# Optimization experiments

Measured on AMD Instinct MI355X. Metric: run time of the kernel, lower is better.

Reference implementation:

```python
import math
import jax, jax.numpy as jnp
import numpy as np

B, S, D, H, KV = 2, 2048, 1024, 16, 4
HD = D // H  # 64
ROPE_BASE = 10000.0
RMS_EPS = 1.1920929e-07  # torch.finfo(float32).eps, F.rms_norm default


def setup_inputs() -> dict:
    key = jax.random.key(0)
    ks = jax.random.split(key, 5)
    x = jax.random.normal(ks[0], (B, S, D), jnp.float32)
    Wq = jax.random.normal(ks[1], (D, D), jnp.float32) * 0.02
    Wk = jax.random.normal(ks[2], (KV * HD, D), jnp.float32) * 0.02
    Wv = jax.random.normal(ks[3], (KV * HD, D), jnp.float32) * 0.02
    Wproj = jax.random.normal(ks[4], (D, D), jnp.float32) * 0.02
    q_gain = jnp.ones((H,), jnp.float32)  # qk_gain_init = 1.0
    return {"x": x, "Wq": Wq, "Wk": Wk, "Wv": Wv, "Wproj": Wproj, "q_gain": q_gain}


def _rms_norm(t):
    # F.rms_norm with no weight: t * rsqrt(mean(t^2) + eps)
    return t * jax.lax.rsqrt(jnp.mean(t * t, axis=-1, keepdims=True) + RMS_EPS)


def _rope(t, cos, sin):
    half = t.shape[-1] // 2
    t1, t2 = t[..., :half], t[..., half:]
    return jnp.concatenate([t1 * cos + t2 * sin, t1 * -sin + t2 * cos], axis=-1)


def reference(x, Wq, Wk, Wv, Wproj, q_gain):
    bsz, seqlen, dim = x.shape
    hd = dim // H
    # QKV projections (Linear weight layout [out, in])
    q = (x @ Wq.T).reshape(bsz, seqlen, H, hd).transpose(0, 2, 1, 3)    # [B,H,S,hd]
    k = (x @ Wk.T).reshape(bsz, seqlen, KV, hd).transpose(0, 2, 1, 3)   # [B,KV,S,hd]
    v = (x @ Wv.T).reshape(bsz, seqlen, KV, hd).transpose(0, 2, 1, 3)
    # per-head RMSNorm on q/k (no learned weight)
    q = _rms_norm(q)
    k = _rms_norm(k)
    # RoPE tables
    inv_freq = 1.0 / (ROPE_BASE ** (jnp.arange(0, hd, 2, dtype=jnp.float32) / hd))
    t = jnp.arange(seqlen, dtype=jnp.float32)
    freqs = t[:, None] * inv_freq[None, :]                              # [S, hd/2]
    cos = jnp.cos(freqs)[None, None]                                    # [1,1,S,hd/2]
    sin = jnp.sin(freqs)[None, None]
    q = _rope(q, cos, sin)
    k = _rope(k, cos, sin)
    # learned per-head query gain
    q = q * q_gain[None, :, None, None]
    # GQA: repeat_interleave kv heads to full head count
    rep = H // KV
    k = jnp.repeat(k, rep, axis=1)                                      # [B,H,S,hd]
    v = jnp.repeat(v, rep, axis=1)
    # causal SDPA, scale = 1/sqrt(head_dim)
    scores = jnp.einsum("bhqd,bhkd->bhqk", q, k) * (1.0 / math.sqrt(hd))
    causal = jnp.tril(jnp.ones((seqlen, seqlen), bool))
    scores = jnp.where(causal[None, None], scores, jnp.finfo(scores.dtype).min)
    attn = jax.nn.softmax(scores, axis=-1)
    y = jnp.einsum("bhqk,bhkd->bhqd", attn, v)
    y = y.transpose(0, 2, 1, 3).reshape(bsz, seqlen, dim)
    return y @ Wproj.T
```

## Files before the change

kernel.cpp:

```cpp
#include <hip/hip_runtime.h>

typedef unsigned short u16;
typedef __bf16 bf16_t;
typedef bf16_t bf16x8 __attribute__((ext_vector_type(8)));
typedef float f32x4 __attribute__((ext_vector_type(4)));
typedef u16 u16x8 __attribute__((ext_vector_type(8)));

__device__ __forceinline__ u16 f2bf(float f) {
  unsigned u = __float_as_uint(f);
  u += 0x7fffu + ((u >> 16) & 1u);
  return (u16)(u >> 16);
}

__device__ __forceinline__ unsigned cvtpk(float lo, float hi) {
  unsigned r;
  asm("v_cvt_pk_bf16_f32 %0, %1, %2" : "=v"(r) : "v"(lo), "v"(hi));
  return r;
}

__device__ __forceinline__ f32x4 mfma16(bf16x8 a, bf16x8 b, f32x4 c) {
  return __builtin_amdgcn_mfma_f32_16x16x32_bf16(a, b, c, 0, 0, 0);
}

__device__ __forceinline__ void gl2lds16(const u16* g, u16* l) {
  __builtin_amdgcn_global_load_lds(
      (__attribute__((address_space(1))) void*)(u16*)g,
      (__attribute__((address_space(3))) void*)l, 16, 0, 0);
}

__device__ __forceinline__ void cast8(const float* __restrict__ in,
                                      u16* __restrict__ out, int i) {
  float4 a = *(const float4*)&in[i];
  float4 b = *(const float4*)&in[i + 4];
  uint4 o;
  o.x = cvtpk(a.x, a.y);
  o.y = cvtpk(a.z, a.w);
  o.z = cvtpk(b.x, b.y);
  o.w = cvtpk(b.z, b.w);
  *(uint4*)&out[i] = o;
}

__global__ __launch_bounds__(256) void megacast(
    const float* __restrict__ x, const float* __restrict__ Wq,
    const float* __restrict__ Wk, const float* __restrict__ Wv,
    const float* __restrict__ Wp, u16* __restrict__ xb,
    u16* __restrict__ wallb, u16* __restrict__ wpb,
    float2* __restrict__ tbl) {
  const int blk = blockIdx.x;
  const int tid = threadIdx.x;
  if (blk < 2048) {
    cast8(x, xb, (blk * 256 + tid) * 8);
  } else if (blk < 2560) {
    cast8(Wq, wallb, ((blk - 2048) * 256 + tid) * 8);
  } else if (blk < 2688) {
    cast8(Wk, wallb + 1048576, ((blk - 2560) * 256 + tid) * 8);
  } else if (blk < 2816) {
    cast8(Wv, wallb + 1310720, ((blk - 2688) * 256 + tid) * 8);
  } else if (blk < 3328) {
    cast8(Wp, wpb, ((blk - 2816) * 256 + tid) * 8);
  } else {
    const int idx = (blk - 3328) * 256 + tid;
    const int s = idx >> 5, i = idx & 31;
    float inv = exp2f(-(float)i * (13.287712379549449f / 32.0f));
    float fr = (float)s * inv;
    float sn, cs;
    sincosf(fr, &sn, &cs);
    tbl[idx] = make_float2(cs, sn);
  }
}

template <int BM, int BN, int NTN, bool O16>
__global__ __launch_bounds__(256) void gemm_bt(const u16* __restrict__ A,
                                               const u16* __restrict__ B,
                                               void* __restrict__ Cv,
                                               int M, int N, int K) {
  constexpr int FM = BM / 32;
  constexpr int FN = BN / 32;
  constexpr int NL = (BM + BN) / 32;
  __shared__ __align__(16) u16 As[2][BM][64];
  __shared__ __align__(16) u16 Bs[2][BN][64];
  const int tid = threadIdx.x;
  const int lane = tid & 63;
  const int lg = lane >> 4, li = lane & 15;
  const int wave = tid >> 6;
  const int wr = (wave >> 1) * (BM / 2), wc = (wave & 1) * (BN / 2);
  const int wid = (blockIdx.x & 7) * (gridDim.x >> 3) + (blockIdx.x >> 3);
  const int m0 = (wid / NTN) * BM, n0 = (wid % NTN) * BN;

  const int s_r = tid >> 3;
  const int s_c = (tid & 7) ^ ((tid >> 3) & 7);
  const int rdsw = li & 7;

  auto GSTAGE = [&](int buf, int k0) {
    const u16* ga = &A[(size_t)(m0 + s_r) * K + k0 + s_c * 8];
#pragma unroll
    for (int i = 0; i < BM / 32; i++)
      gl2lds16(ga + (size_t)(i * 32) * K, &As[buf][i * 32][0] + (size_t)tid * 8);
    const u16* gb = &B[(size_t)(n0 + s_r) * K + k0 + s_c * 8];
#pragma unroll
    for (int i = 0; i < BN / 32; i++)
      gl2lds16(gb + (size_t)(i * 32) * K, &Bs[buf][i * 32][0] + (size_t)tid * 8);
  };

  const f32x4 fz = {0.f, 0.f, 0.f, 0.f};
  f32x4 acc[FM][FN];
#pragma unroll
  for (int i = 0; i < FM; i++)
#pragma unroll
    for (int j = 0; j < FN; j++) acc[i][j] = fz;

  GSTAGE(0, 0);
  int buf = 0;
  const int nk = K >> 6;
  for (int t = 0; t < nk; ++t) {
    if (t + 1 < nk) {
      GSTAGE(buf ^ 1, (t + 1) * 64);
      if constexpr (NL == 6)
        asm volatile("s_waitcnt vmcnt(6)" ::: "memory");
      else
        asm volatile("s_waitcnt vmcnt(8)" ::: "memory");
    } else {
      asm volatile("s_waitcnt vmcnt(0)" ::: "memory");
    }
    __builtin_amdgcn_s_barrier();
#pragma unroll
    for (int kk = 0; kk < 2; kk++) {
      bf16x8 af[FM], bfr[FN];
#pragma unroll
      for (int i = 0; i < FM; i++)
        af[i] = *(const bf16x8*)&As[buf][wr + i * 16 + li]
                                   [((kk * 4 + lg) ^ rdsw) * 8];
#pragma unroll
      for (int j = 0; j < FN; j++)
        bfr[j] = *(const bf16x8*)&Bs[buf][wc + j * 16 + li]
                                    [((kk * 4 + lg) ^ rdsw) * 8];
      __builtin_amdgcn_s_setprio(1);
#pragma unroll
      for (int i = 0; i < FM; i++)
#pragma unroll
        for (int j = 0; j < FN; j++) acc[i][j] = mfma16(af[i], bfr[j], acc[i][j]);
      __builtin_amdgcn_s_setprio(0);
    }
    __builtin_amdgcn_s_barrier();
    buf ^= 1;
  }
#pragma unroll
  for (int i = 0; i < FM; i++)
#pragma unroll
    for (int j = 0; j < FN; j++)
#pragma unroll
      for (int r = 0; r < 4; r++) {
        const size_t idx =
            (size_t)(m0 + wr + i * 16 + lg * 4 + r) * N + n0 + wc + j * 16 + li;
        if constexpr (O16)
          ((u16*)Cv)[idx] = f2bf(acc[i][j][r]);
        else
          ((float*)Cv)[idx] = acc[i][j][r];
      }
}

__global__ __launch_bounds__(256) void gemm_qkv(const u16* __restrict__ A,
                                                const u16* __restrict__ B,
                                                const float* __restrict__ qg,
                                                u16* __restrict__ qhb,
                                                u16* __restrict__ khb,
                                                u16* __restrict__ vtb,
                                                const float2* __restrict__ tbl) {
  const int K = 1024, S = 2048;
  __shared__ __align__(16) u16 As[2][128][64];
  __shared__ __align__(16) u16 Bs[2][64][64];
  const int tid = threadIdx.x;
  const int lane = tid & 63;
  const int lg = lane >> 4, li = lane & 15;
  const int wave = tid >> 6;
  const int wr = (wave >> 1) * 64, wc = (wave & 1) * 32;
  const int wid = (blockIdx.x & 7) * 96 + (blockIdx.x >> 3);
  const int mt = wid / 24;
  const int ntile = wid - mt * 24;
  const int m0 = mt * 128;

  const int s_r = tid >> 3;
  const int s_c = (tid & 7) ^ ((tid >> 3) & 7);
  const int rdsw = li & 7;

  auto GSTAGE = [&](int buf, int k0) {
    const u16* ga = &A[(size_t)(m0 + s_r) * K + k0 + s_c * 8];
#pragma unroll
    for (int i = 0; i < 4; i++)
      gl2lds16(ga + (size_t)(i * 32) * K, &As[buf][i * 32][0] + (size_t)tid * 8);
    const u16* gb = &B[(size_t)(ntile * 64 + s_r) * K + k0 + s_c * 8];
#pragma unroll
    for (int i = 0; i < 2; i++)
      gl2lds16(gb + (size_t)(i * 32) * K, &Bs[buf][i * 32][0] + (size_t)tid * 8);
  };

  const f32x4 fz = {0.f, 0.f, 0.f, 0.f};
  f32x4 acc[4][2];
#pragma unroll
  for (int i = 0; i < 4; i++)
#pragma unroll
    for (int j = 0; j < 2; j++) acc[i][j] = fz;

  GSTAGE(0, 0);
  int buf = 0;
  for (int t = 0; t < 16; ++t) {
    if (t + 1 < 16) {
      GSTAGE(buf ^ 1, (t + 1) * 64);
      asm volatile("s_waitcnt vmcnt(6)" ::: "memory");
    } else {
      asm volatile("s_waitcnt vmcnt(0)" ::: "memory");
    }
    __builtin_amdgcn_s_barrier();
#pragma unroll
    for (int kk = 0; kk < 2; kk++) {
      bf16x8 af[4], bfr[2];
#pragma unroll
      for (int i = 0; i < 4; i++)
        af[i] = *(const bf16x8*)&As[buf][wr + i * 16 + li]
                                   [((kk * 4 + lg) ^ rdsw) * 8];
#pragma unroll
      for (int j = 0; j < 2; j++)
        bfr[j] = *(const bf16x8*)&Bs[buf][wc + j * 16 + li]
                                    [((kk * 4 + lg) ^ rdsw) * 8];
      __builtin_amdgcn_s_setprio(1);
#pragma unroll
      for (int i = 0; i < 4; i++)
#pragma unroll
        for (int j = 0; j < 2; j++) acc[i][j] = mfma16(af[i], bfr[j], acc[i][j]);
      __builtin_amdgcn_s_setprio(0);
    }
    __builtin_amdgcn_s_barrier();
    buf ^= 1;
  }

  if (ntile < 20) {
    float* acc_t = (float*)&As[0][0][0];
    float* sw = (float*)&Bs[0][0][0];
    float ssq[4][4];
#pragma unroll
    for (int i = 0; i < 4; i++)
#pragma unroll
      for (int r = 0; r < 4; r++) {
        float s2 = acc[i][0][r] * acc[i][0][r] + acc[i][1][r] * acc[i][1][r];
        s2 += __shfl_xor(s2, 1);
        s2 += __shfl_xor(s2, 2);
        s2 += __shfl_xor(s2, 4);
        s2 += __shfl_xor(s2, 8);
        ssq[i][r] = s2;
        const int rowidx = i * 16 + lg * 4 + r;
        if (li == 0) sw[wave * 64 + rowidx] = s2;
#pragma unroll
        for (int j = 0; j < 2; j++)
          acc_t[wave * 2048 + rowidx * 32 + j * 16 + li] = acc[i][j][r];
      }
    __syncthreads();
    const int pw = wave ^ 1;
    const float qsc =
        (ntile < 16) ? 0.18033688011112042f * qg[ntile] : 1.0f;
#pragma unroll
    for (int i = 0; i < 4; i++)
#pragma unroll
      for (int r = 0; r < 4; r++) {
        const int rowidx = i * 16 + lg * 4 + r;
        const float stot = ssq[i][r] + sw[pw * 64 + rowidx];
        const float rn = rsqrtf(stot * (1.0f / 64.0f) + 1.1920929e-07f);
        const int grow = m0 + wr + rowidx;
        const int srow = grow & 2047;
        const int bb = grow >> 11;
#pragma unroll
        for (int j = 0; j < 2; j++) {
          const int fi = j * 16 + li;
          const float2 cs2 = tbl[srow * 32 + fi];
          const float vn = acc[i][j][r] * rn;
          const float pvn = acc_t[pw * 2048 + rowidx * 32 + fi] * rn;
          float o = (wc == 0) ? (vn * cs2.x + pvn * cs2.y)
                              : (vn * cs2.x - pvn * cs2.y);
          o *= qsc;
          const int col = wc + fi;
          if (ntile < 16)
            qhb[((size_t)(bb * 16 + ntile) * S + srow) * 64 + col] = f2bf(o);
          else
            khb[((size_t)(bb * 4 + (ntile - 16)) * S + srow) * 64 + col] =
                f2bf(o);
        }
      }
  } else {
    u16* T = (u16*)&As[0][0][0];
#pragma unroll
    for (int i = 0; i < 4; i++)
#pragma unroll
      for (int j = 0; j < 2; j++)
#pragma unroll
        for (int r = 0; r < 4; r++)
          T[(wr + i * 16 + lg * 4 + r) * 67 + wc + j * 16 + li] =
              f2bf(acc[i][j][r]);
    __syncthreads();
    const int kv = ntile - 20;
    const int d = tid >> 2;
    const int sq = (tid & 3) * 32;
    const int bb = m0 >> 11;
    const int s0 = (m0 & 2047) + sq;
    unsigned* dst = (unsigned*)(vtb + ((size_t)(bb * 4 + kv) * 64 + d) * S + s0);
#pragma unroll
    for (int k2 = 0; k2 < 16; k2++) {
      unsigned lo = T[(sq + 2 * k2) * 67 + d];
      unsigned hi = T[(sq + 2 * k2 + 1) * 67 + d];
      dst[k2] = lo | (hi << 16);
    }
  }
}

__global__ __launch_bounds__(256) void attn13(const u16* __restrict__ qh,
                                              const u16* __restrict__ kh,
                                              const u16* __restrict__ vt,
                                              const float* __restrict__ qg,
                                              u16* __restrict__ y, int S) {
  const int bh = blockIdx.x & 31;
  const int g = blockIdx.x >> 5;
  const int d = g & 7, u = g >> 3;
  const int qb = (u == 0) ? 31 - d : (u == 1) ? 16 + d : (u == 2) ? 15 - d : d;
  const int h = bh & 15, b = bh >> 4;
  const int kvh = h >> 2;
  const int tid = threadIdx.x;
  const int wave = tid >> 6;
  const int lane = tid & 63;
  const int lg = lane >> 4, li = lane & 15;
  const int q0 = qb * 64 + wave * 16;
  const int qrow = q0 + li;
  const float mrow = 11.541560327111707f * fabsf(qg[h]);

  const u16* qp = qh + ((size_t)(b * 16 + h) * S + q0) * 64;
  const u16* kp = kh + (size_t)(b * 4 + kvh) * S * 64;
  const u16* vp = vt + (size_t)(b * 4 + kvh) * 64 * S;

  __shared__ __align__(16) u16 Ks[2][64][64];
  __shared__ __align__(16) u16 Vs[2][64][64];

  const int s_r0 = tid >> 3;
  const int s_rp = (s_r0 & ~24) | ((s_r0 & 8) << 1) | ((s_r0 & 16) >> 1);
  const int s_c = (tid & 7) ^ ((tid >> 3) & 7);
  const int rdsw = li & 7;
  const f32x4 minit = {-mrow, -mrow, -mrow, -mrow};
  const f32x4 fz = {0.f, 0.f, 0.f, 0.f};
  const u16x8 ones_u = {0x3F80, 0x3F80, 0x3F80, 0x3F80,
                        0x3F80, 0x3F80, 0x3F80, 0x3F80};
  const bf16x8 onesb = *(const bf16x8*)&ones_u;

#define STAGE(buf, kb)                                                        \
  {                                                                           \
    const u16* gk = kp + (size_t)((kb) + s_rp) * 64 + s_c * 8;                \
    gl2lds16(gk, &Ks[buf][0][0] + (size_t)tid * 8);                           \
    gl2lds16(gk + (size_t)32 * 64, &Ks[buf][32][0] + (size_t)tid * 8);        \
    const u16* gv = vp + (size_t)s_r0 * S + (kb) + s_c * 8;                   \
    gl2lds16(gv, &Vs[buf][0][0] + (size_t)tid * 8);                           \
    gl2lds16(gv + (size_t)32 * S, &Vs[buf][32][0] + (size_t)tid * 8);         \
  }

  STAGE(0, 0)
  const bf16x8 qf0 = *(const bf16x8*)&qp[li * 64 + lg * 8];
  const bf16x8 qf1 = *(const bf16x8*)&qp[li * 64 + 32 + lg * 8];

  f32x4 o[4];
#pragma unroll
  for (int j = 0; j < 4; j++) o[j] = fz;
  f32x4 lsum = fz;

  int buf = 0;
  for (int tt = 0; tt <= qb; ++tt) {
    if (tt < qb) {
      STAGE(buf ^ 1, (tt + 1) * 64)
      asm volatile("s_waitcnt vmcnt(4)" ::: "memory");
    } else {
      asm volatile("s_waitcnt vmcnt(0)" ::: "memory");
    }
    __builtin_amdgcn_s_barrier();
    const int kb = tt * 64;
    f32x4 s[4];
    __builtin_amdgcn_s_setprio(1);
#pragma unroll
    for (int t = 0; t < 4; t++) {
      const bf16x8 ka =
          *(const bf16x8*)&Ks[buf][t * 16 + li][((lg) ^ rdsw) * 8];
      const bf16x8 kc =
          *(const bf16x8*)&Ks[buf][t * 16 + li][((lg + 4) ^ rdsw) * 8];
      s[t] = mfma16(ka, qf0, minit);
      s[t] = mfma16(kc, qf1, s[t]);
    }
    __builtin_amdgcn_s_setprio(0);
    float pv[16];
    if (tt < qb) {
#pragma unroll
      for (int t = 0; t < 4; t++)
#pragma unroll
        for (int r = 0; r < 4; r++) pv[t * 4 + r] = exp2f(s[t][r]);
    } else {
#pragma unroll
      for (int t = 0; t < 4; t++)
#pragma unroll
        for (int r = 0; r < 4; r++) {
          const int key = kb + ((t >> 1) << 5) + ((lg & 2) << 3) +
                          ((t & 1) << 3) + ((lg & 1) << 2) + r;
          pv[t * 4 + r] = exp2f(key > qrow ? -1e30f : s[t][r]);
        }
    }
    unsigned w0 = cvtpk(pv[0], pv[1]),   w1 = cvtpk(pv[2], pv[3]);
    unsigned w2 = cvtpk(pv[4], pv[5]),   w3 = cvtpk(pv[6], pv[7]);
    unsigned w4 = cvtpk(pv[8], pv[9]),   w5 = cvtpk(pv[10], pv[11]);
    unsigned w6 = cvtpk(pv[12], pv[13]), w7 = cvtpk(pv[14], pv[15]);
    asm("v_permlane16_swap_b32 %0, %1" : "+v"(w0), "+v"(w2));
    asm("v_permlane16_swap_b32 %0, %1" : "+v"(w1), "+v"(w3));
    asm("v_permlane16_swap_b32 %0, %1" : "+v"(w4), "+v"(w6));
    asm("v_permlane16_swap_b32 %0, %1" : "+v"(w5), "+v"(w7));
    uint4 pb0u = {w0, w1, w2, w3};
    uint4 pb1u = {w4, w5, w6, w7};
    const bf16x8 pb0 = *(const bf16x8*)&pb0u;
    const bf16x8 pb1 = *(const bf16x8*)&pb1u;
    __builtin_amdgcn_s_setprio(1);
#pragma unroll
    for (int j = 0; j < 4; j++) {
      const bf16x8 v0 =
          *(const bf16x8*)&Vs[buf][j * 16 + li][((lg) ^ rdsw) * 8];
      const bf16x8 v1 =
          *(const bf16x8*)&Vs[buf][j * 16 + li][((lg + 4) ^ rdsw) * 8];
      o[j] = mfma16(v0, pb0, o[j]);
      o[j] = mfma16(v1, pb1, o[j]);
    }
    lsum = mfma16(onesb, pb0, lsum);
    lsum = mfma16(onesb, pb1, lsum);
    __builtin_amdgcn_s_setprio(0);
    __builtin_amdgcn_s_barrier();
    buf ^= 1;
  }
#undef STAGE
  const float linv = 1.0f / lsum[0];
  u16* yp = &y[((size_t)(b * S + q0 + li)) * 1024 + h * 64];
#pragma unroll
  for (int j = 0; j < 4; j++) {
    uint2 wo;
    wo.x = cvtpk(o[j][0] * linv, o[j][1] * linv);
    wo.y = cvtpk(o[j][2] * linv, o[j][3] * linv);
    *(uint2*)(yp + j * 16 + lg * 4) = wo;
  }
}

extern "C" void kernel_launch(void* const* d_in, const int* in_sizes, int n_in,
                              void* d_out, int out_size, void* d_ws, size_t ws_size,
                              hipStream_t stream) {
  const float* x  = (const float*)d_in[0];
  const float* Wq = (const float*)d_in[1];
  const float* Wk = (const float*)d_in[2];
  const float* Wv = (const float*)d_in[3];
  const float* Wp = (const float*)d_in[4];
  const float* qg = (const float*)d_in[5];
  float* out = (float*)d_out;

  const int S = 2048;
  char* ws = (char*)d_ws;
  u16*    xb    = (u16*)(ws + 0);
  u16*    wallb = (u16*)(ws + 8388608);
  u16*    wpb   = (u16*)(ws + 11534336);
  float2* tbl   = (float2*)(ws + 13631488);
  u16*    qhb   = (u16*)(ws + 14155776);
  u16*    khb   = (u16*)(ws + 22544384);
  u16*    vtb   = (u16*)(ws + 24641536);
  u16*    yb    = (u16*)(ws + 26738688);
  if (ws_size < 35127296) return;

  megacast<<<3584, 256, 0, stream>>>(x, Wq, Wk, Wv, Wp, xb, wallb, wpb, tbl);

  gemm_qkv<<<768, 256, 0, stream>>>(xb, wallb, qg, qhb, khb, vtb, tbl);

  attn13<<<1024, 256, 0, stream>>>(qhb, khb, vtb, qg, yb, S);

  gemm_bt<64, 128, 8, false><<<512, 256, 0, stream>>>(yb, wpb, out,
                                                      4096, 1024, 1024);
}
```

Before: 90.24 us.

## Merge four causal query tiles into one 1024-thread attention block sharing K/V stages

Restructures the attention kernel so each 1024-thread block handles four 64-row query tiles (d, 15-d, 16+d, 31-d) of the same head, sharing a single K/V LDS staging stream. Each K/V tile is loaded once per block instead of once per query tile, which cuts global and L2 traffic, and pairing the tiles this way balances causal work across blocks. In exchange the grid shrinks to 256 blocks, and waves whose query tile is finished sit idle at the barriers while the later tiles keep going. Large blocks may also reduce occupancy flexibility.

New measurement: 91.38 us. No clear change (+1.3%).

```diff
diff --git a/kernel.cpp b/kernel.cpp
--- a/kernel.cpp
+++ b/kernel.cpp
@@ -310,22 +310,23 @@
   }
 }
 
-__global__ __launch_bounds__(256) void attn13(const u16* __restrict__ qh,
-                                              const u16* __restrict__ kh,
-                                              const u16* __restrict__ vt,
-                                              const float* __restrict__ qg,
-                                              u16* __restrict__ y, int S) {
+__global__ __launch_bounds__(1024) void attn16(const u16* __restrict__ qh,
+                                               const u16* __restrict__ kh,
+                                               const u16* __restrict__ vt,
+                                               const float* __restrict__ qg,
+                                               u16* __restrict__ y, int S) {
   const int bh = blockIdx.x & 31;
-  const int g = blockIdx.x >> 5;
-  const int d = g & 7, u = g >> 3;
-  const int qb = (u == 0) ? 31 - d : (u == 1) ? 16 + d : (u == 2) ? 15 - d : d;
+  const int d = blockIdx.x >> 5;
   const int h = bh & 15, b = bh >> 4;
   const int kvh = h >> 2;
   const int tid = threadIdx.x;
   const int wave = tid >> 6;
   const int lane = tid & 63;
   const int lg = lane >> 4, li = lane & 15;
-  const int q0 = qb * 64 + wave * 16;
+  const int wg = wave >> 2;
+  const int qt = (wg == 0) ? d : (wg == 1) ? 15 - d : (wg == 2) ? 16 + d
+                                                                : 31 - d;
+  const int q0 = qt * 64 + (wave & 3) * 16;
   const int qrow = q0 + li;
   const float mrow = 11.541560327111707f * fabsf(qg[h]);
 
@@ -336,9 +337,11 @@
   __shared__ __align__(16) u16 Ks[2][64][64];
   __shared__ __align__(16) u16 Vs[2][64][64];
 
-  const int s_r0 = tid >> 3;
-  const int s_rp = (s_r0 & ~24) | ((s_r0 & 8) << 1) | ((s_r0 & 16) >> 1);
-  const int s_c = (tid & 7) ^ ((tid >> 3) & 7);
+  const bool isK = tid < 512;
+  const int t2 = isK ? tid : tid - 512;
+  const int srow = t2 >> 3;
+  const int s_c = (t2 & 7) ^ (srow & 7);
+  const int srowp = (srow & ~24) | ((srow & 8) << 1) | ((srow & 16) >> 1);
   const int rdsw = li & 7;
   const f32x4 minit = {-mrow, -mrow, -mrow, -mrow};
   const f32x4 fz = {0.f, 0.f, 0.f, 0.f};
@@ -348,12 +351,12 @@
 
 #define STAGE(buf, kb)                                                        \
   {                                                                           \
-    const u16* gk = kp + (size_t)((kb) + s_rp) * 64 + s_c * 8;                \
-    gl2lds16(gk, &Ks[buf][0][0] + (size_t)tid * 8);                           \
-    gl2lds16(gk + (size_t)32 * 64, &Ks[buf][32][0] + (size_t)tid * 8);        \
-    const u16* gv = vp + (size_t)s_r0 * S + (kb) + s_c * 8;                   \
-    gl2lds16(gv, &Vs[buf][0][0] + (size_t)tid * 8);                           \
-    gl2lds16(gv + (size_t)32 * S, &Vs[buf][32][0] + (size_t)tid * 8);         \
+    if (isK)                                                                  \
+      gl2lds16(kp + (size_t)((kb) + srowp) * 64 + s_c * 8,                    \
+               &Ks[buf][0][0] + (size_t)t2 * 8);                              \
+    else                                                                      \
+      gl2lds16(vp + (size_t)srow * S + (kb) + s_c * 8,                        \
+               &Vs[buf][0][0] + (size_t)t2 * 8);                              \
   }
 
   STAGE(0, 0)
@@ -365,69 +368,72 @@
   for (int j = 0; j < 4; j++) o[j] = fz;
   f32x4 lsum = fz;
 
+  const int nkv = 32 - d;
   int buf = 0;
-  for (int tt = 0; tt <= qb; ++tt) {
-    if (tt < qb) {
+  for (int tt = 0; tt < nkv; ++tt) {
+    if (tt + 1 < nkv) {
       STAGE(buf ^ 1, (tt + 1) * 64)
-      asm volatile("s_waitcnt vmcnt(4)" ::: "memory");
+      asm volatile("s_waitcnt vmcnt(1)" ::: "memory");
     } else {
       asm volatile("s_waitcnt vmcnt(0)" ::: "memory");
     }
     __builtin_amdgcn_s_barrier();
-    const int kb = tt * 64;
-    f32x4 s[4];
-    __builtin_amdgcn_s_setprio(1);
-#pragma unroll
-    for (int t = 0; t < 4; t++) {
-      const bf16x8 ka =
-          *(const bf16x8*)&Ks[buf][t * 16 + li][((lg) ^ rdsw) * 8];
-      const bf16x8 kc =
-          *(const bf16x8*)&Ks[buf][t * 16 + li][((lg + 4) ^ rdsw) * 8];
-      s[t] = mfma16(ka, qf0, minit);
-      s[t] = mfma16(kc, qf1, s[t]);
-    }
-    __builtin_amdgcn_s_setprio(0);
-    float pv[16];
-    if (tt < qb) {
-#pragma unroll
-      for (int t = 0; t < 4; t++)
-#pragma unroll
-        for (int r = 0; r < 4; r++) pv[t * 4 + r] = exp2f(s[t][r]);
-    } else {
-#pragma unroll
-      for (int t = 0; t < 4; t++)
-#pragma unroll
-        for (int r = 0; r < 4; r++) {
-          const int key = kb + ((t >> 1) << 5) + ((lg & 2) << 3) +
-                          ((t & 1) << 3) + ((lg & 1) << 2) + r;
-          pv[t * 4 + r] = exp2f(key > qrow ? -1e30f : s[t][r]);
-        }
-    }
-    unsigned w0 = cvtpk(pv[0], pv[1]),   w1 = cvtpk(pv[2], pv[3]);
-    unsigned w2 = cvtpk(pv[4], pv[5]),   w3 = cvtpk(pv[6], pv[7]);
-    unsigned w4 = cvtpk(pv[8], pv[9]),   w5 = cvtpk(pv[10], pv[11]);
-    unsigned w6 = cvtpk(pv[12], pv[13]), w7 = cvtpk(pv[14], pv[15]);
-    asm("v_permlane16_swap_b32 %0, %1" : "+v"(w0), "+v"(w2));
-    asm("v_permlane16_swap_b32 %0, %1" : "+v"(w1), "+v"(w3));
-    asm("v_permlane16_swap_b32 %0, %1" : "+v"(w4), "+v"(w6));
-    asm("v_permlane16_swap_b32 %0, %1" : "+v"(w5), "+v"(w7));
-    uint4 pb0u = {w0, w1, w2, w3};
-    uint4 pb1u = {w4, w5, w6, w7};
-    const bf16x8 pb0 = *(const bf16x8*)&pb0u;
-    const bf16x8 pb1 = *(const bf16x8*)&pb1u;
-    __builtin_amdgcn_s_setprio(1);
-#pragma unroll
-    for (int j = 0; j < 4; j++) {
-      const bf16x8 v0 =
-          *(const bf16x8*)&Vs[buf][j * 16 + li][((lg) ^ rdsw) * 8];
-      const bf16x8 v1 =
-          *(const bf16x8*)&Vs[buf][j * 16 + li][((lg + 4) ^ rdsw) * 8];
-      o[j] = mfma16(v0, pb0, o[j]);
-      o[j] = mfma16(v1, pb1, o[j]);
-    }
-    lsum = mfma16(onesb, pb0, lsum);
-    lsum = mfma16(onesb, pb1, lsum);
-    __builtin_amdgcn_s_setprio(0);
+    if (tt <= qt) {
+      const int kb = tt * 64;
+      f32x4 s[4];
+      __builtin_amdgcn_s_setprio(1);
+#pragma unroll
+      for (int t = 0; t < 4; t++) {
+        const bf16x8 ka =
+            *(const bf16x8*)&Ks[buf][t * 16 + li][((lg) ^ rdsw) * 8];
+        const bf16x8 kc =
+            *(const bf16x8*)&Ks[buf][t * 16 + li][((lg + 4) ^ rdsw) * 8];
+        s[t] = mfma16(ka, qf0, minit);
+        s[t] = mfma16(kc, qf1, s[t]);
+      }
+      __builtin_amdgcn_s_setprio(0);
+      float pv[16];
+      if (tt < qt) {
+#pragma unroll
+        for (int t = 0; t < 4; t++)
+#pragma unroll
+          for (int r = 0; r < 4; r++) pv[t * 4 + r] = exp2f(s[t][r]);
+      } else {
+#pragma unroll
+        for (int t = 0; t < 4; t++)
+#pragma unroll
+          for (int r = 0; r < 4; r++) {
+            const int key = kb + ((t >> 1) << 5) + ((lg & 2) << 3) +
+                            ((t & 1) << 3) + ((lg & 1) << 2) + r;
+            pv[t * 4 + r] = exp2f(key > qrow ? -1e30f : s[t][r]);
+          }
+      }
+      unsigned w0 = cvtpk(pv[0], pv[1]),   w1 = cvtpk(pv[2], pv[3]);
+      unsigned w2 = cvtpk(pv[4], pv[5]),   w3 = cvtpk(pv[6], pv[7]);
+      unsigned w4 = cvtpk(pv[8], pv[9]),   w5 = cvtpk(pv[10], pv[11]);
+      unsigned w6 = cvtpk(pv[12], pv[13]), w7 = cvtpk(pv[14], pv[15]);
+      asm("v_permlane16_swap_b32 %0, %1" : "+v"(w0), "+v"(w2));
+      asm("v_permlane16_swap_b32 %0, %1" : "+v"(w1), "+v"(w3));
+      asm("v_permlane16_swap_b32 %0, %1" : "+v"(w4), "+v"(w6));
+      asm("v_permlane16_swap_b32 %0, %1" : "+v"(w5), "+v"(w7));
+      uint4 pb0u = {w0, w1, w2, w3};
+      uint4 pb1u = {w4, w5, w6, w7};
+      const bf16x8 pb0 = *(const bf16x8*)&pb0u;
+      const bf16x8 pb1 = *(const bf16x8*)&pb1u;
+      __builtin_amdgcn_s_setprio(1);
+#pragma unroll
+      for (int j = 0; j < 4; j++) {
+        const bf16x8 v0 =
+            *(const bf16x8*)&Vs[buf][j * 16 + li][((lg) ^ rdsw) * 8];
+        const bf16x8 v1 =
+            *(const bf16x8*)&Vs[buf][j * 16 + li][((lg + 4) ^ rdsw) * 8];
+        o[j] = mfma16(v0, pb0, o[j]);
+        o[j] = mfma16(v1, pb1, o[j]);
+      }
+      lsum = mfma16(onesb, pb0, lsum);
+      lsum = mfma16(onesb, pb1, lsum);
+      __builtin_amdgcn_s_setprio(0);
+    }
     __builtin_amdgcn_s_barrier();
     buf ^= 1;
   }
@@ -470,7 +476,7 @@
 
   gemm_qkv<<<768, 256, 0, stream>>>(xb, wallb, qg, qhb, khb, vtb, tbl);
 
-  attn13<<<1024, 256, 0, stream>>>(qhb, khb, vtb, qg, yb, S);
+  attn16<<<256, 1024, 0, stream>>>(qhb, khb, vtb, qg, yb, S);
 
   gemm_bt<64, 128, 8, false><<<512, 256, 0, stream>>>(yb, wpb, out,
                                                       4096, 1024, 1024);
```

## Fuse x fp32-to-bf16 cast into QKV GEMM A-tile loading

Applied to the files above, without the earlier changes.

Removes the separate conversion of x to bf16 in the cast kernel. The QKV GEMM now loads fp32 x rows into registers, converts them with packed bf16 conversion and writes them to a single LDS A buffer, while B weights still go through direct global-to-LDS loads. This avoids writing and rereading an 8 MB bf16 copy of x. In exchange the GEMM reads twice as many A bytes per tile, holds more registers for prefetched fp32 data, and uses a single-buffered A tile.

Result: slower. 116.9 us (+29.6%).

```diff
diff --git a/kernel.cpp b/kernel.cpp
--- a/kernel.cpp
+++ b/kernel.cpp
@@ -41,25 +41,21 @@
 }
 
 __global__ __launch_bounds__(256) void megacast(
-    const float* __restrict__ x, const float* __restrict__ Wq,
-    const float* __restrict__ Wk, const float* __restrict__ Wv,
-    const float* __restrict__ Wp, u16* __restrict__ xb,
-    u16* __restrict__ wallb, u16* __restrict__ wpb,
-    float2* __restrict__ tbl) {
+    const float* __restrict__ Wq, const float* __restrict__ Wk,
+    const float* __restrict__ Wv, const float* __restrict__ Wp,
+    u16* __restrict__ wallb, u16* __restrict__ wpb, float2* __restrict__ tbl) {
   const int blk = blockIdx.x;
   const int tid = threadIdx.x;
-  if (blk < 2048) {
-    cast8(x, xb, (blk * 256 + tid) * 8);
-  } else if (blk < 2560) {
-    cast8(Wq, wallb, ((blk - 2048) * 256 + tid) * 8);
-  } else if (blk < 2688) {
-    cast8(Wk, wallb + 1048576, ((blk - 2560) * 256 + tid) * 8);
-  } else if (blk < 2816) {
-    cast8(Wv, wallb + 1310720, ((blk - 2688) * 256 + tid) * 8);
-  } else if (blk < 3328) {
-    cast8(Wp, wpb, ((blk - 2816) * 256 + tid) * 8);
+  if (blk < 512) {
+    cast8(Wq, wallb, (blk * 256 + tid) * 8);
+  } else if (blk < 640) {
+    cast8(Wk, wallb + 1048576, ((blk - 512) * 256 + tid) * 8);
+  } else if (blk < 768) {
+    cast8(Wv, wallb + 1310720, ((blk - 640) * 256 + tid) * 8);
+  } else if (blk < 1280) {
+    cast8(Wp, wpb, ((blk - 768) * 256 + tid) * 8);
   } else {
-    const int idx = (blk - 3328) * 256 + tid;
+    const int idx = (blk - 1280) * 256 + tid;
     const int s = idx >> 5, i = idx & 31;
     float inv = exp2f(-(float)i * (13.287712379549449f / 32.0f));
     float fr = (float)s * inv;
@@ -159,16 +155,17 @@
       }
 }
 
-__global__ __launch_bounds__(256) void gemm_qkv(const u16* __restrict__ A,
-                                                const u16* __restrict__ B,
+__global__ __launch_bounds__(256) void gemm_qkv(const float* __restrict__ X,
+                                                const u16* __restrict__ Bw,
                                                 const float* __restrict__ qg,
                                                 u16* __restrict__ qhb,
                                                 u16* __restrict__ khb,
                                                 u16* __restrict__ vtb,
                                                 const float2* __restrict__ tbl) {
   const int K = 1024, S = 2048;
-  __shared__ __align__(16) u16 As[2][128][64];
-  __shared__ __align__(16) u16 Bs[2][64][64];
+  __shared__ __align__(16) u16 pool[17536];
+  u16* Asl = pool;
+  u16* Bsl = pool + 8192;
   const int tid = threadIdx.x;
   const int lane = tid & 63;
   const int lg = lane >> 4, li = lane & 15;
@@ -183,16 +180,34 @@
   const int s_c = (tid & 7) ^ ((tid >> 3) & 7);
   const int rdsw = li & 7;
 
-  auto GSTAGE = [&](int buf, int k0) {
-    const u16* ga = &A[(size_t)(m0 + s_r) * K + k0 + s_c * 8];
-#pragma unroll
-    for (int i = 0; i < 4; i++)
-      gl2lds16(ga + (size_t)(i * 32) * K, &As[buf][i * 32][0] + (size_t)tid * 8);
-    const u16* gb = &B[(size_t)(ntile * 64 + s_r) * K + k0 + s_c * 8];
-#pragma unroll
-    for (int i = 0; i < 2; i++)
-      gl2lds16(gb + (size_t)(i * 32) * K, &Bs[buf][i * 32][0] + (size_t)tid * 8);
-  };
+  const float* ga = X + (size_t)(m0 + s_r) * K + s_c * 8;
+  const u16* gb0 = Bw + (size_t)(ntile * 64 + s_r) * K + s_c * 8;
+
+#define LOADA(dst, k0)                                                        \
+  {                                                                           \
+    _Pragma("unroll") for (int i = 0; i < 4; i++) {                           \
+      dst[2 * i] = *(const float4*)(ga + (size_t)(i * 32) * K + (k0));        \
+      dst[2 * i + 1] =                                                        \
+          *(const float4*)(ga + (size_t)(i * 32) * K + (k0) + 4);             \
+    }                                                                         \
+  }
+#define STAGEB(buf, k0)                                                       \
+  {                                                                           \
+    gl2lds16(gb0 + (k0), Bsl + (size_t)(buf)*4096 + (size_t)tid * 8);         \
+    gl2lds16(gb0 + (size_t)32 * K + (k0),                                     \
+             Bsl + (size_t)(buf)*4096 + 32 * 64 + (size_t)tid * 8);           \
+  }
+#define WRITEA(src)                                                           \
+  {                                                                           \
+    _Pragma("unroll") for (int i = 0; i < 4; i++) {                           \
+      uint4 w;                                                                \
+      w.x = cvtpk(src[2 * i].x, src[2 * i].y);                                \
+      w.y = cvtpk(src[2 * i].z, src[2 * i].w);                                \
+      w.z = cvtpk(src[2 * i + 1].x, src[2 * i + 1].y);                        \
+      w.w = cvtpk(src[2 * i + 1].z, src[2 * i + 1].w);                        \
+      *(uint4*)(Asl + (size_t)(i * 32) * 64 + (size_t)tid * 8) = w;           \
+    }                                                                         \
+  }
 
   const f32x4 fz = {0.f, 0.f, 0.f, 0.f};
   f32x4 acc[4][2];
@@ -201,41 +216,54 @@
 #pragma unroll
     for (int j = 0; j < 2; j++) acc[i][j] = fz;
 
-  GSTAGE(0, 0);
+  float4 aA[8], aB[8];
+  LOADA(aA, 0)
+  STAGEB(0, 0)
   int buf = 0;
-  for (int t = 0; t < 16; ++t) {
-    if (t + 1 < 16) {
-      GSTAGE(buf ^ 1, (t + 1) * 64);
-      asm volatile("s_waitcnt vmcnt(6)" ::: "memory");
-    } else {
-      asm volatile("s_waitcnt vmcnt(0)" ::: "memory");
-    }
-    __builtin_amdgcn_s_barrier();
-#pragma unroll
-    for (int kk = 0; kk < 2; kk++) {
-      bf16x8 af[4], bfr[2];
-#pragma unroll
-      for (int i = 0; i < 4; i++)
-        af[i] = *(const bf16x8*)&As[buf][wr + i * 16 + li]
-                                   [((kk * 4 + lg) ^ rdsw) * 8];
-#pragma unroll
-      for (int j = 0; j < 2; j++)
-        bfr[j] = *(const bf16x8*)&Bs[buf][wc + j * 16 + li]
-                                    [((kk * 4 + lg) ^ rdsw) * 8];
-      __builtin_amdgcn_s_setprio(1);
-#pragma unroll
-      for (int i = 0; i < 4; i++)
-#pragma unroll
-        for (int j = 0; j < 2; j++) acc[i][j] = mfma16(af[i], bfr[j], acc[i][j]);
-      __builtin_amdgcn_s_setprio(0);
-    }
-    __builtin_amdgcn_s_barrier();
-    buf ^= 1;
-  }
+
+#define QKV_BODY(t, CUR, NXT)                                                 \
+  {                                                                           \
+    if ((t) + 1 < 16) {                                                       \
+      LOADA(NXT, ((t) + 1) * 64)                                              \
+      STAGEB(buf ^ 1, ((t) + 1) * 64)                                         \
+    }                                                                         \
+    WRITEA(CUR)                                                               \
+    if ((t) + 1 < 16)                                                         \
+      asm volatile("s_waitcnt vmcnt(10) lgkmcnt(0)" ::: "memory");            \
+    else                                                                      \
+      asm volatile("s_waitcnt vmcnt(0) lgkmcnt(0)" ::: "memory");             \
+    __builtin_amdgcn_s_barrier();                                             \
+    _Pragma("unroll") for (int kk = 0; kk < 2; kk++) {                        \
+      bf16x8 af[4], bfr[2];                                                   \
+      _Pragma("unroll") for (int i = 0; i < 4; i++) af[i] =                   \
+          *(const bf16x8*)(Asl + (size_t)(wr + i * 16 + li) * 64 +            \
+                           ((kk * 4 + lg) ^ rdsw) * 8);                       \
+      _Pragma("unroll") for (int j = 0; j < 2; j++) bfr[j] =                  \
+          *(const bf16x8*)(Bsl + (size_t)buf * 4096 +                         \
+                           (size_t)(wc + j * 16 + li) * 64 +                  \
+                           ((kk * 4 + lg) ^ rdsw) * 8);                       \
+      __builtin_amdgcn_s_setprio(1);                                          \
+      _Pragma("unroll") for (int i = 0; i < 4; i++)                           \
+          _Pragma("unroll") for (int j = 0; j < 2; j++) acc[i][j] =           \
+              mfma16(af[i], bfr[j], acc[i][j]);                               \
+      __builtin_amdgcn_s_setprio(0);                                          \
+    }                                                                         \
+    __builtin_amdgcn_s_barrier();                                             \
+    buf ^= 1;                                                                 \
+  }
+
+  for (int t = 0; t < 16; t += 2) {
+    QKV_BODY(t, aA, aB)
+    QKV_BODY(t + 1, aB, aA)
+  }
+#undef QKV_BODY
+#undef LOADA
+#undef STAGEB
+#undef WRITEA
 
   if (ntile < 20) {
-    float* acc_t = (float*)&As[0][0][0];
-    float* sw = (float*)&Bs[0][0][0];
+    float* acc_t = (float*)pool;
+    float* sw = (float*)(pool + 16384);
     float ssq[4][4];
 #pragma unroll
     for (int i = 0; i < 4; i++)
@@ -285,7 +313,7 @@
         }
       }
   } else {
-    u16* T = (u16*)&As[0][0][0];
+    u16* T = pool;
 #pragma unroll
     for (int i = 0; i < 4; i++)
 #pragma unroll
@@ -456,19 +484,18 @@
 
   const int S = 2048;
   char* ws = (char*)d_ws;
-  u16*    xb    = (u16*)(ws + 0);
-  u16*    wallb = (u16*)(ws + 8388608);
-  u16*    wpb   = (u16*)(ws + 11534336);
-  float2* tbl   = (float2*)(ws + 13631488);
-  u16*    qhb   = (u16*)(ws + 14155776);
-  u16*    khb   = (u16*)(ws + 22544384);
-  u16*    vtb   = (u16*)(ws + 24641536);
-  u16*    yb    = (u16*)(ws + 26738688);
-  if (ws_size < 35127296) return;
-
-  megacast<<<3584, 256, 0, stream>>>(x, Wq, Wk, Wv, Wp, xb, wallb, wpb, tbl);
-
-  gemm_qkv<<<768, 256, 0, stream>>>(xb, wallb, qg, qhb, khb, vtb, tbl);
+  u16*    wallb = (u16*)(ws + 0);
+  u16*    wpb   = (u16*)(ws + 3145728);
+  float2* tbl   = (float2*)(ws + 5242880);
+  u16*    qhb   = (u16*)(ws + 5767168);
+  u16*    khb   = (u16*)(ws + 14155776);
+  u16*    vtb   = (u16*)(ws + 16252928);
+  u16*    yb    = (u16*)(ws + 18350080);
+  if (ws_size < 26738688) return;
+
+  megacast<<<1536, 256, 0, stream>>>(Wq, Wk, Wv, Wp, wallb, wpb, tbl);
+
+  gemm_qkv<<<768, 256, 0, stream>>>(x, wallb, qg, qhb, khb, vtb, tbl);
 
   attn13<<<1024, 256, 0, stream>>>(qhb, khb, vtb, qg, yb, S);
 
```
